# Performance work log

Measured on AMD Instinct MI355X. Metric: run time of the kernel, lower is better.

Reference implementation:

```python
import jax, jax.numpy as jnp
import numpy as np

B, S, H = 1, 2048, 1024          # batch, seq, hidden_size
INTER, K, DST, DTR = 2048, 4, 16, 64  # intermediate, kernel, ssm_state, dt_rank


def setup_inputs() -> dict:
    key = jax.random.key(0)
    ks = jax.random.split(key, 10)
    sc = 0.02
    return {
        "x": jax.random.normal(ks[0], (B, S, H), jnp.float32),
        "W_in": jax.random.normal(ks[1], (H, 2 * INTER), jnp.float32) * sc,
        "conv_w": jax.random.normal(ks[2], (K, 1, INTER), jnp.float32) * sc,
        "conv_b": jax.random.normal(ks[3], (INTER,), jnp.float32) * sc,
        "W_x": jax.random.normal(ks[4], (INTER, DTR + 2 * DST), jnp.float32) * sc,
        "W_dt": jax.random.normal(ks[5], (DTR, INTER), jnp.float32) * sc,
        "b_dt": jax.random.normal(ks[6], (INTER,), jnp.float32) * sc,
        "A_log": jax.random.normal(ks[7], (INTER, DST), jnp.float32) * sc,
        "D": jax.random.normal(ks[8], (INTER,), jnp.float32) * sc,
        "W_out": jax.random.normal(ks[9], (INTER, H), jnp.float32) * sc,
    }


def _ssm(dA, dBu, C):
    # dA, dBu: (b, s, h, d); C: (b, s, d) -> y: (b, s, h)
    xs = (jnp.moveaxis(dA, 1, 0), jnp.moveaxis(dBu, 1, 0), jnp.moveaxis(C, 1, 0))
    state0 = jnp.zeros(dA.shape[:1] + dA.shape[2:], dA.dtype)  # (b, h, d)

    def step(state, inp):
        Ai, dBui, Ci = inp  # (b,h,d), (b,h,d), (b,d)
        state = Ai * state + dBui
        y = jnp.einsum('bhd,bd->bh', state, Ci)
        return state, y

    _, ys = jax.lax.scan(step, state0, xs)  # ys: (s, b, h)
    return jnp.moveaxis(ys, 0, 1)


def reference(x, W_in, conv_w, conv_b, W_x, W_dt, b_dt, A_log, D, W_out):
    proj = x @ W_in                              # (b, s, 2*inter)
    raw, gate = jnp.split(proj, 2, axis=-1)      # each (b, s, inter)

    # causal depthwise conv over time, groups = inter
    conv = jax.lax.conv_general_dilated(
        raw, conv_w, window_strides=(1,), padding=[(K - 1, 0)],
        dimension_numbers=('NWC', 'WIO', 'NWC'), feature_group_count=INTER)
    h = jax.nn.silu(conv + conv_b)               # (b, s, inter)

    ssm_p = h @ W_x                              # (b, s, dtr + 2*d)
    ts, Bmat, C = jnp.split(ssm_p, [DTR, DTR + DST], axis=-1)
    dt = jax.nn.softplus(ts @ W_dt + b_dt)       # (b, s, inter)

    A = -jnp.exp(A_log)                          # (inter, d)
    dA = jnp.exp(dt[..., None] * A)              # (b, s, inter, d)
    dBu = dt[..., None] * Bmat[:, :, None, :] * h[..., None]  # (b, s, inter, d)

    y = _ssm(dA, dBu, C)                         # (b, s, inter)
    y = y + h * D
    y = y * jax.nn.silu(gate)
    return y @ W_out                             # (b, s, hidden)
```

## Files before the change

### kernel.cpp

```cpp
#include <hip/hip_runtime.h>
#include <math.h>

#define SEQ   2048
#define HID   1024
#define INTER 2048
#define DST   16
#define DTR   64
#define NP    96
#define NC    128
#define LCH   16
#define KS    16

typedef _Float16 f16;
typedef _Float16 f16x8 __attribute__((ext_vector_type(8)));
typedef _Float16 f16x4v __attribute__((ext_vector_type(4)));
typedef float f32x4 __attribute__((ext_vector_type(4)));

__device__ __forceinline__ float sigmoidf_(float x) { return 1.0f / (1.0f + expf(-x)); }
__device__ __forceinline__ float siluf_(float x)    { return x * sigmoidf_(x); }
__device__ __forceinline__ float softplusf_(float x){ return (x > 20.0f) ? x : log1pf(expf(x)); }

__device__ __forceinline__ int xcd_swz(int bid, int nwg)
{
    int cpx = nwg >> 3;
    return (bid & 7) * cpx + (bid >> 3);
}

__device__ __forceinline__ void tile_transpose(const float* __restrict__ W,
                                               f16* __restrict__ Wt,
                                               int K, int N, int bx, int by, int tid)
{
    __shared__ float t[32][33];
    const int n0 = bx * 32, k0 = by * 32;
    const int j = tid & 31, i0 = tid >> 5;
#pragma unroll
    for (int r = 0; r < 4; ++r)
        t[i0 + r * 8][j] = W[(size_t)(k0 + i0 + r * 8) * N + n0 + j];
    __syncthreads();
#pragma unroll
    for (int r = 0; r < 4; ++r)
        Wt[(size_t)(n0 + i0 + r * 8) * K + k0 + j] = (f16)t[j][i0 + r * 8];
}

__global__ __launch_bounds__(256) void prep_all(const float* __restrict__ x,
                                                const float* __restrict__ W_in,
                                                const float* __restrict__ W_out,
                                                const float* __restrict__ W_x,
                                                const float* __restrict__ W_dt,
                                                f16* __restrict__ xh,
                                                f16* __restrict__ W_in_t,
                                                f16* __restrict__ W_out_t,
                                                f16* __restrict__ WxT,
                                                f16* __restrict__ WdtT)
{
    const int bid = blockIdx.x, tid = threadIdx.x;
    if (bid < 2048) {
        int i = (bid * 256 + tid) * 4;
        float4 v = *(const float4*)&x[i];
        f16x4v o;
        o.x = (f16)v.x; o.y = (f16)v.y; o.z = (f16)v.z; o.w = (f16)v.w;
        *(f16x4v*)&xh[i] = o;
    } else if (bid < 6144) {
        int t = bid - 2048;
        tile_transpose(W_in, W_in_t, HID, 4096, t & 127, t >> 7, tid);
    } else if (bid < 8192) {
        int t = bid - 6144;
        tile_transpose(W_out, W_out_t, INTER, HID, t & 31, t >> 5, tid);
    } else if (bid < 8384) {
        int t = bid - 8192;
        tile_transpose(W_x, WxT, INTER, NP, t % 3, t / 3, tid);
    } else {
        int t = bid - 8384;
        tile_transpose(W_dt, WdtT, DTR, INTER, t & 63, t >> 6, tid);
    }
}

template<int BM, int BN, int KK, typename OutT>
__global__ __launch_bounds__(256) void gemm_f16mfma(const f16* __restrict__ Ah,
                                                    const f16* __restrict__ Bt,
                                                    OutT* __restrict__ C,
                                                    int N, int nbx)
{
    constexpr int BK = 64;
    __shared__ __align__(16) f16 As[BM * BK];
    __shared__ __align__(16) f16 Bs[BN * BK];

    const int tile = xcd_swz(blockIdx.x, gridDim.x);
    const int bx = tile % nbx, by = tile / nbx;

    const int tid = threadIdx.x;
    const int wid = tid >> 6, lane = tid & 63;
    const int wr = wid >> 1, wc = wid & 1;
    const int m0 = by * BM, n0 = bx * BN;
    const int l15 = lane & 15, lhi = lane >> 4;

    constexpr int MR = BM / 32;
    constexpr int NR = BN / 32;

    f32x4 acc[MR][NR] = {};

    for (int k0 = 0; k0 < KK; k0 += BK) {
        constexpr int CA = BM * BK * 2 / 1024;
#pragma unroll
        for (int c0 = 0; c0 < CA; c0 += 4) {
            int c = c0 + wid;
            int e = c * 64 + lane;
            int row = e >> 3, seg = e & 7;
            __builtin_amdgcn_global_load_lds(
                (const __attribute__((address_space(1))) unsigned int*)
                    (Ah + (size_t)(m0 + row) * KK + k0 + seg * 8),
                (__attribute__((address_space(3))) unsigned int*)(As + c * 512),
                16, 0, 0);
        }
        constexpr int CB = BN * BK * 2 / 1024;
#pragma unroll
        for (int c0 = 0; c0 < CB; c0 += 4) {
            int c = c0 + wid;
            int e = c * 64 + lane;
            int row = e >> 3, seg = e & 7;
            __builtin_amdgcn_global_load_lds(
                (const __attribute__((address_space(1))) unsigned int*)
                    (Bt + (size_t)(n0 + row) * KK + k0 + seg * 8),
                (__attribute__((address_space(3))) unsigned int*)(Bs + c * 512),
                16, 0, 0);
        }
        __syncthreads();

#pragma unroll
        for (int kk = 0; kk < BK; kk += 32) {
            f16x8 af[MR], bf[NR];
#pragma unroll
            for (int i = 0; i < MR; ++i)
                af[i] = *(const f16x8*)&As[(wr * (BM / 2) + i * 16 + l15) * BK + kk + lhi * 8];
#pragma unroll
            for (int n = 0; n < NR; ++n)
                bf[n] = *(const f16x8*)&Bs[(wc * (BN / 2) + n * 16 + l15) * BK + kk + lhi * 8];
#pragma unroll
            for (int i = 0; i < MR; ++i)
#pragma unroll
                for (int n = 0; n < NR; ++n)
                    acc[i][n] = __builtin_amdgcn_mfma_f32_16x16x32_f16(af[i], bf[n], acc[i][n], 0, 0, 0);
        }
        __syncthreads();
    }

#pragma unroll
    for (int i = 0; i < MR; ++i)
#pragma unroll
        for (int n = 0; n < NR; ++n)
#pragma unroll
            for (int r = 0; r < 4; ++r)
                C[(size_t)(m0 + wr * (BM / 2) + i * 16 + lhi * 4 + r) * N
                  + n0 + wc * (BN / 2) + n * 16 + l15] = (OutT)acc[i][n][r];
}

__global__ __launch_bounds__(256) void hwx_mfma(const f16* __restrict__ hh,
                                                const f16* __restrict__ WxT,
                                                f16* __restrict__ partials)
{
    constexpr int BM = 128, BN = 96, BK = 64;
    __shared__ __align__(16) f16 As[BM * BK];
    __shared__ __align__(16) f16 Bs[BN * BK];

    const int tile = xcd_swz(blockIdx.x, gridDim.x);
    const int bxm = tile & 15, ks = tile >> 4;

    const int tid = threadIdx.x;
    const int wid = tid >> 6, lane = tid & 63;
    const int wr = wid >> 1, wc = wid & 1;
    const int m0 = bxm * BM;
    const int l15 = lane & 15, lhi = lane >> 4;

    constexpr int MR = 4, NR = 3;
    f32x4 acc[MR][NR] = {};

    for (int k0 = ks * 128; k0 < ks * 128 + 128; k0 += BK) {
#pragma unroll
        for (int c0 = 0; c0 < 16; c0 += 4) {
            int c = c0 + wid;
            int e = c * 64 + lane;
            int row = e >> 3, seg = e & 7;
            __builtin_amdgcn_global_load_lds(
                (const __attribute__((address_space(1))) unsigned int*)
                    (hh + (size_t)(m0 + row) * INTER + k0 + seg * 8),
                (__attribute__((address_space(3))) unsigned int*)(As + c * 512),
                16, 0, 0);
        }
#pragma unroll
        for (int c0 = 0; c0 < 12; c0 += 4) {
            int c = c0 + wid;
            int e = c * 64 + lane;
            int row = e >> 3, seg = e & 7;
            __builtin_amdgcn_global_load_lds(
                (const __attribute__((address_space(1))) unsigned int*)
                    (WxT + (size_t)row * INTER + k0 + seg * 8),
                (__attribute__((address_space(3))) unsigned int*)(Bs + c * 512),
                16, 0, 0);
        }
        __syncthreads();

#pragma unroll
        for (int kk = 0; kk < BK; kk += 32) {
            f16x8 af[MR], bf[NR];
#pragma unroll
            for (int i = 0; i < MR; ++i)
                af[i] = *(const f16x8*)&As[(wr * 64 + i * 16 + l15) * BK + kk + lhi * 8];
#pragma unroll
            for (int n = 0; n < NR; ++n)
                bf[n] = *(const f16x8*)&Bs[(wc * 48 + n * 16 + l15) * BK + kk + lhi * 8];
#pragma unroll
            for (int i = 0; i < MR; ++i)
#pragma unroll
                for (int n = 0; n < NR; ++n)
                    acc[i][n] = __builtin_amdgcn_mfma_f32_16x16x32_f16(af[i], bf[n], acc[i][n], 0, 0, 0);
        }
        __syncthreads();
    }

    f16* P = partials + (size_t)ks * (SEQ * NP);
#pragma unroll
    for (int i = 0; i < MR; ++i)
#pragma unroll
        for (int n = 0; n < NR; ++n)
#pragma unroll
            for (int r = 0; r < 4; ++r)
                P[(size_t)(m0 + wr * 64 + i * 16 + lhi * 4 + r) * NP
                  + wc * 48 + n * 16 + l15] = (f16)acc[i][n][r];
}

__global__ __launch_bounds__(256) void reduce_partials(const f16* __restrict__ partials,
                                                       float* __restrict__ ssm_p,
                                                       f16* __restrict__ tsh)
{
    int t = blockIdx.x * 256 + threadIdx.x;
    int i8 = t * 8;
    int s = i8 / NP, j0 = i8 % NP;
    float a[8] = {};
#pragma unroll
    for (int c = 0; c < KS; ++c) {
        f16x8 v = *(const f16x8*)&partials[(size_t)c * (SEQ * NP) + i8];
#pragma unroll
        for (int j = 0; j < 8; ++j) a[j] += (float)v[j];
    }
    if (j0 < DTR) {
        f16x8 o;
#pragma unroll
        for (int j = 0; j < 8; ++j) o[j] = (f16)a[j];
        *(f16x8*)&tsh[(size_t)s * DTR + j0] = o;
    } else {
        *(float4*)&ssm_p[(size_t)s * NP + j0]     = make_float4(a[0], a[1], a[2], a[3]);
        *(float4*)&ssm_p[(size_t)s * NP + j0 + 4] = make_float4(a[4], a[5], a[6], a[7]);
    }
}

__global__ __launch_bounds__(256) void dt_mfma(const f16* __restrict__ tsh,
                                               const f16* __restrict__ WdtT,
                                               const float* __restrict__ bdt,
                                               f16* __restrict__ dtbh)
{
    constexpr int BM = 128, BN = 128, BK = 64;
    __shared__ __align__(16) f16 As[BM * BK];
    __shared__ __align__(16) f16 Bs[BN * BK];

    const int tile = xcd_swz(blockIdx.x, gridDim.x);
    const int bx = tile & 15, by = tile >> 4;

    const int tid = threadIdx.x;
    const int wid = tid >> 6, lane = tid & 63;
    const int wr = wid >> 1, wc = wid & 1;
    const int m0 = by * BM, n0 = bx * BN;
    const int l15 = lane & 15, lhi = lane >> 4;

    constexpr int MR = 4, NR = 4;
    f32x4 acc[MR][NR] = {};

#pragma unroll
    for (int c0 = 0; c0 < 16; c0 += 4) {
        int c = c0 + wid;
        int e = c * 64 + lane;
        int row = e >> 3, seg = e & 7;
        __builtin_amdgcn_global_load_lds(
            (const __attribute__((address_space(1))) unsigned int*)
                (tsh + (size_t)(m0 + row) * DTR + seg * 8),
            (__attribute__((address_space(3))) unsigned int*)(As + c * 512),
            16, 0, 0);
        __builtin_amdgcn_global_load_lds(
            (const __attribute__((address_space(1))) unsigned int*)
                (WdtT + (size_t)(n0 + row) * DTR + seg * 8),
            (__attribute__((address_space(3))) unsigned int*)(Bs + c * 512),
            16, 0, 0);
    }
    __syncthreads();

#pragma unroll
    for (int kk = 0; kk < 64; kk += 32) {
        f16x8 af[MR], bf[NR];
#pragma unroll
        for (int i = 0; i < MR; ++i)
            af[i] = *(const f16x8*)&As[(wr * 64 + i * 16 + l15) * BK + kk + lhi * 8];
#pragma unroll
        for (int n = 0; n < NR; ++n)
            bf[n] = *(const f16x8*)&Bs[(wc * 64 + n * 16 + l15) * BK + kk + lhi * 8];
#pragma unroll
        for (int i = 0; i < MR; ++i)
#pragma unroll
            for (int n = 0; n < NR; ++n)
                acc[i][n] = __builtin_amdgcn_mfma_f32_16x16x32_f16(af[i], bf[n], acc[i][n], 0, 0, 0);
    }

#pragma unroll
    for (int i = 0; i < MR; ++i)
#pragma unroll
        for (int n = 0; n < NR; ++n) {
            int col = n0 + wc * 64 + n * 16 + l15;
            float bv = bdt[col];
#pragma unroll
            for (int r = 0; r < 4; ++r)
                dtbh[(size_t)(m0 + wr * 64 + i * 16 + lhi * 4 + r) * INTER + col] =
                    (f16)softplusf_(acc[i][n][r] + bv);
        }
}

__global__ __launch_bounds__(256) void conv_silu(const f16* __restrict__ projh,
                                                 const float* __restrict__ cw,
                                                 const float* __restrict__ cb,
                                                 f16* __restrict__ hh)
{
    int idx = blockIdx.x * 256 + threadIdx.x;
    int c8 = (idx & (INTER / 8 - 1)) * 8;
    int s = idx >> 8;
    float acc[8];
#pragma unroll
    for (int j = 0; j < 8; ++j) acc[j] = cb[c8 + j];
#pragma unroll
    for (int k = 0; k < 4; ++k) {
        int sp = s + k - 3;
        if (sp >= 0) {
            f16x8 p = *(const f16x8*)&projh[(size_t)sp * (2 * INTER) + c8];
#pragma unroll
            for (int j = 0; j < 8; ++j)
                acc[j] = fmaf((float)p[j], cw[k * INTER + c8 + j], acc[j]);
        }
    }
    f16x8 o;
#pragma unroll
    for (int j = 0; j < 8; ++j) o[j] = (f16)siluf_(acc[j]);
    *(f16x8*)&hh[(size_t)idx * 8] = o;
}

__global__ __launch_bounds__(256) void ssm_pass1(const f16* __restrict__ dtbh,
                                                 const f16* __restrict__ hh,
                                                 const float* __restrict__ ssm_p,
                                                 const float* __restrict__ A_log,
                                                 float* __restrict__ Sbuf,
                                                 float* __restrict__ Pbuf)
{
    const int h = blockIdx.x * 256 + threadIdx.x;
    const int c = blockIdx.y;
    const int s0 = c * LCH;

    __shared__ float Bs[LCH][DST];
    for (int j = threadIdx.x; j < LCH * DST; j += 256) {
        int r = j >> 4, dd = j & 15;
        Bs[r][dd] = ssm_p[(size_t)(s0 + r) * NP + DTR + dd];
    }
    __syncthreads();

    float A[DST], st[DST];
#pragma unroll
    for (int d = 0; d < DST; ++d) {
        A[d] = -__expf(A_log[(size_t)h * DST + d]);
        st[d] = 0.0f;
    }

    float dtsum = 0.0f;
    for (int r = 0; r < LCH; ++r) {
        float dtv = (float)dtbh[(size_t)(s0 + r) * INTER + h];
        float hv  = (float)hh[(size_t)(s0 + r) * INTER + h];
        float dh = dtv * hv;
        dtsum += dtv;
#pragma unroll
        for (int d = 0; d < DST; ++d) {
            float da = __expf(dtv * A[d]);
            st[d] = fmaf(da, st[d], dh * Bs[r][d]);
        }
    }

    size_t base = ((size_t)c * INTER + h) * DST;
#pragma unroll
    for (int d = 0; d < DST; d += 4) {
        *(float4*)&Sbuf[base + d] = make_float4(st[d], st[d+1], st[d+2], st[d+3]);
        float4 p4;
        p4.x = __expf(A[d]     * dtsum);
        p4.y = __expf(A[d + 1] * dtsum);
        p4.z = __expf(A[d + 2] * dtsum);
        p4.w = __expf(A[d + 3] * dtsum);
        *(float4*)&Pbuf[base + d] = p4;
    }
}

__global__ __launch_bounds__(256) void ssm_pass2(const float* __restrict__ Sbuf,
                                                 const float* __restrict__ Pbuf,
                                                 float* __restrict__ Cin)
{
    int i = blockIdx.x * 256 + threadIdx.x;
    float carry = 0.0f;
#pragma unroll 8
    for (int c = 0; c < NC; ++c) {
        size_t idx = (size_t)c * (INTER * DST) + i;
        Cin[idx] = carry;
        carry = fmaf(Pbuf[idx], carry, Sbuf[idx]);
    }
}

__global__ __launch_bounds__(256) void ssm_pass3(const f16* __restrict__ dtbh,
                                                 const f16* __restrict__ hh,
                                                 const float* __restrict__ ssm_p,
                                                 const f16* __restrict__ projh,
                                                 const float* __restrict__ A_log,
                                                 const float* __restrict__ Dvec,
                                                 const float* __restrict__ Cin,
                                                 f16* __restrict__ yh)
{
    const int h = blockIdx.x * 256 + threadIdx.x;
    const int c = blockIdx.y;
    const int s0 = c * LCH;

    __shared__ float Bs[LCH][DST];
    __shared__ float Cs[LCH][DST];
    for (int j = threadIdx.x; j < LCH * DST; j += 256) {
        int r = j >> 4, dd = j & 15;
        Bs[r][dd] = ssm_p[(size_t)(s0 + r) * NP + DTR + dd];
        Cs[r][dd] = ssm_p[(size_t)(s0 + r) * NP + DTR + DST + dd];
    }
    __syncthreads();

    float A[DST], st[DST];
    size_t base = ((size_t)c * INTER + h) * DST;
#pragma unroll
    for (int d = 0; d < DST; ++d) {
        A[d] = -__expf(A_log[(size_t)h * DST + d]);
        st[d] = Cin[base + d];
    }
    const float Dv = Dvec[h];

    for (int r = 0; r < LCH; ++r) {
        float dtv = (float)dtbh[(size_t)(s0 + r) * INTER + h];
        float hv  = (float)hh[(size_t)(s0 + r) * INTER + h];
        float g   = (float)projh[(size_t)(s0 + r) * (2 * INTER) + INTER + h];
        float dh = dtv * hv;
        float y = 0.0f;
#pragma unroll
        for (int d = 0; d < DST; ++d) {
            float da = __expf(dtv * A[d]);
            st[d] = fmaf(da, st[d], dh * Bs[r][d]);
            y = fmaf(st[d], Cs[r][d], y);
        }
        y = fmaf(hv, Dv, y);
        yh[(size_t)(s0 + r) * INTER + h] = (f16)(y * siluf_(g));
    }
}

extern "C" void kernel_launch(void* const* d_in, const int* in_sizes, int n_in,
                              void* d_out, int out_size, void* d_ws, size_t ws_size,
                              hipStream_t stream)
{
    const float* x      = (const float*)d_in[0];
    const float* W_in   = (const float*)d_in[1];
    const float* conv_w = (const float*)d_in[2];
    const float* conv_b = (const float*)d_in[3];
    const float* W_x    = (const float*)d_in[4];
    const float* W_dt   = (const float*)d_in[5];
    const float* b_dt   = (const float*)d_in[6];
    const float* A_log  = (const float*)d_in[7];
    const float* Dv     = (const float*)d_in[8];
    const float* W_out  = (const float*)d_in[9];
    float* out = (float*)d_out;

    float* ws = (float*)d_ws;
    f16*  projh  = (f16*)ws;
    f16*  hh     = (f16*)(ws + 4194304);
    f16*  dtbh   = (f16*)(ws + 6291456);
    f16*  yh     = (f16*)(ws + 8388608);
    f16*  xh     = (f16*)(ws + 10485760);
    f16*  W_in_t = (f16*)(ws + 11534336);
    f16*  W_out_t= (f16*)(ws + 13631488);
    f16*  WxT    = (f16*)(ws + 14680064);
    f16*  tsh    = (f16*)(ws + 14778368);
    f16*  WdtT   = (f16*)(ws + 14843904);
    float* ssm_p = ws + 14909440;
    f16*  parts  = (f16*)(ws + 15106048);
    float* Sbuf  = ws + 16678912;
    float* Pbuf  = ws + 20873216;
    float* Cin   = ws + 25067520;

    prep_all<<<8512, 256, 0, stream>>>(x, W_in, W_out, W_x, W_dt,
                                       xh, W_in_t, W_out_t, WxT, WdtT);

    gemm_f16mfma<128, 128, HID, f16><<<512, 256, 0, stream>>>(
        xh, W_in_t, projh, 2 * INTER, 32);

    conv_silu<<<(SEQ * INTER / 8) / 256, 256, 0, stream>>>(projh, conv_w, conv_b, hh);

    hwx_mfma<<<256, 256, 0, stream>>>(hh, WxT, parts);
    reduce_partials<<<(SEQ * NP / 8) / 256, 256, 0, stream>>>(parts, ssm_p, tsh);

    dt_mfma<<<256, 256, 0, stream>>>(tsh, WdtT, b_dt, dtbh);

    ssm_pass1<<<dim3(INTER / 256, NC), 256, 0, stream>>>(dtbh, hh, ssm_p, A_log, Sbuf, Pbuf);
    ssm_pass2<<<(INTER * DST) / 256, 256, 0, stream>>>(Sbuf, Pbuf, Cin);
    ssm_pass3<<<dim3(INTER / 256, NC), 256, 0, stream>>>(dtbh, hh, ssm_p, projh, A_log, Dv, Cin, yh);

    gemm_f16mfma<64, 128, INTER, float><<<256, 256, 0, stream>>>(
        yh, W_out_t, out, HID, 8);
}
```

Baseline: 183.0 us.

## Split-K both projection GEMMs and fold partial reduction into conv and output passes

Both large GEMMs now use a split-K of 2, writing f16 partial planes, which doubles the number of workgroups (1024 and 512) so more compute units are filled. The in-projection partials are summed inside a new conv_gate kernel that also writes a separate gate buffer. The out-projection partials are summed by a new reduce_out kernel. The SSM chunking changes to 64 chunks of 32 steps. In exchange the partial planes add extra memory traffic, one extra launch, and an extra f16 rounding of the partial sums.

```diff
diff --git a/kernel.cpp b/kernel.cpp
--- a/kernel.cpp
+++ b/kernel.cpp
@@ -7,8 +7,8 @@
 #define DST   16
 #define DTR   64
 #define NP    96
-#define NC    128
-#define LCH   16
+#define NC    64
+#define LCH   32
 #define KS    16
 
 typedef _Float16 f16;
@@ -75,18 +75,21 @@
     }
 }
 
-template<int BM, int BN, int KK, typename OutT>
-__global__ __launch_bounds__(256) void gemm_f16mfma(const f16* __restrict__ Ah,
-                                                    const f16* __restrict__ Bt,
-                                                    OutT* __restrict__ C,
-                                                    int N, int nbx)
+template<int BM, int BN, int KTOT, int KCH>
+__global__ __launch_bounds__(256) void gemm_sk_f16(const f16* __restrict__ Ah,
+                                                   const f16* __restrict__ Bt,
+                                                   f16* __restrict__ planes,
+                                                   int N, int nbx, int nby)
 {
     constexpr int BK = 64;
     __shared__ __align__(16) f16 As[BM * BK];
     __shared__ __align__(16) f16 Bs[BN * BK];
 
     const int tile = xcd_swz(blockIdx.x, gridDim.x);
-    const int bx = tile % nbx, by = tile / nbx;
+    const int bx = tile % nbx;
+    const int rem = tile / nbx;
+    const int by = rem % nby;
+    const int ks = rem / nby;
 
     const int tid = threadIdx.x;
     const int wid = tid >> 6, lane = tid & 63;
@@ -99,7 +102,7 @@
 
     f32x4 acc[MR][NR] = {};
 
-    for (int k0 = 0; k0 < KK; k0 += BK) {
+    for (int k0 = ks * KCH; k0 < ks * KCH + KCH; k0 += BK) {
         constexpr int CA = BM * BK * 2 / 1024;
 #pragma unroll
         for (int c0 = 0; c0 < CA; c0 += 4) {
@@ -108,7 +111,7 @@
             int row = e >> 3, seg = e & 7;
             __builtin_amdgcn_global_load_lds(
                 (const __attribute__((address_space(1))) unsigned int*)
-                    (Ah + (size_t)(m0 + row) * KK + k0 + seg * 8),
+                    (Ah + (size_t)(m0 + row) * KTOT + k0 + seg * 8),
                 (__attribute__((address_space(3))) unsigned int*)(As + c * 512),
                 16, 0, 0);
         }
@@ -120,7 +123,7 @@
             int row = e >> 3, seg = e & 7;
             __builtin_amdgcn_global_load_lds(
                 (const __attribute__((address_space(1))) unsigned int*)
-                    (Bt + (size_t)(n0 + row) * KK + k0 + seg * 8),
+                    (Bt + (size_t)(n0 + row) * KTOT + k0 + seg * 8),
                 (__attribute__((address_space(3))) unsigned int*)(Bs + c * 512),
                 16, 0, 0);
         }
@@ -144,6 +147,7 @@
         __syncthreads();
     }
 
+    f16* C = planes + (size_t)ks * ((size_t)nby * BM * N);
 #pragma unroll
     for (int i = 0; i < MR; ++i)
 #pragma unroll
@@ -151,7 +155,48 @@
 #pragma unroll
             for (int r = 0; r < 4; ++r)
                 C[(size_t)(m0 + wr * (BM / 2) + i * 16 + lhi * 4 + r) * N
-                  + n0 + wc * (BN / 2) + n * 16 + l15] = (OutT)acc[i][n][r];
+                  + n0 + wc * (BN / 2) + n * 16 + l15] = (f16)acc[i][n][r];
+}
+
+__global__ __launch_bounds__(256) void conv_gate(const f16* __restrict__ pA,
+                                                 const float* __restrict__ cw,
+                                                 const float* __restrict__ cb,
+                                                 f16* __restrict__ hh,
+                                                 f16* __restrict__ gateh)
+{
+    const f16* p1 = pA + (size_t)SEQ * 4096;
+    int idx = blockIdx.x * 256 + threadIdx.x;
+    int cu = idx & 511;
+    int s = idx >> 9;
+    int col = cu * 8;
+    if (col < INTER) {
+        float acc[8];
+#pragma unroll
+        for (int j = 0; j < 8; ++j) acc[j] = cb[col + j];
+#pragma unroll
+        for (int k = 0; k < 4; ++k) {
+            int sp = s + k - 3;
+            if (sp >= 0) {
+                f16x8 a = *(const f16x8*)&pA[(size_t)sp * 4096 + col];
+                f16x8 b = *(const f16x8*)&p1[(size_t)sp * 4096 + col];
+#pragma unroll
+                for (int j = 0; j < 8; ++j)
+                    acc[j] = fmaf((float)a[j] + (float)b[j], cw[k * INTER + col + j], acc[j]);
+            }
+        }
+        f16x8 o;
+#pragma unroll
+        for (int j = 0; j < 8; ++j) o[j] = (f16)siluf_(acc[j]);
+        *(f16x8*)&hh[(size_t)s * INTER + col] = o;
+    } else {
+        int g = col - INTER;
+        f16x8 a = *(const f16x8*)&pA[(size_t)s * 4096 + col];
+        f16x8 b = *(const f16x8*)&p1[(size_t)s * 4096 + col];
+        f16x8 o;
+#pragma unroll
+        for (int j = 0; j < 8; ++j) o[j] = (f16)((float)a[j] + (float)b[j]);
+        *(f16x8*)&gateh[(size_t)s * INTER + g] = o;
+    }
 }
 
 __global__ __launch_bounds__(256) void hwx_mfma(const f16* __restrict__ hh,
@@ -321,33 +366,6 @@
         }
 }
 
-__global__ __launch_bounds__(256) void conv_silu(const f16* __restrict__ projh,
-                                                 const float* __restrict__ cw,
-                                                 const float* __restrict__ cb,
-                                                 f16* __restrict__ hh)
-{
-    int idx = blockIdx.x * 256 + threadIdx.x;
-    int c8 = (idx & (INTER / 8 - 1)) * 8;
-    int s = idx >> 8;
-    float acc[8];
-#pragma unroll
-    for (int j = 0; j < 8; ++j) acc[j] = cb[c8 + j];
-#pragma unroll
-    for (int k = 0; k < 4; ++k) {
-        int sp = s + k - 3;
-        if (sp >= 0) {
-            f16x8 p = *(const f16x8*)&projh[(size_t)sp * (2 * INTER) + c8];
-#pragma unroll
-            for (int j = 0; j < 8; ++j)
-                acc[j] = fmaf((float)p[j], cw[k * INTER + c8 + j], acc[j]);
-        }
-    }
-    f16x8 o;
-#pragma unroll
-    for (int j = 0; j < 8; ++j) o[j] = (f16)siluf_(acc[j]);
-    *(f16x8*)&hh[(size_t)idx * 8] = o;
-}
-
 __global__ __launch_bounds__(256) void ssm_pass1(const f16* __restrict__ dtbh,
                                                  const f16* __restrict__ hh,
                                                  const float* __restrict__ ssm_p,
@@ -416,7 +434,7 @@
 __global__ __launch_bounds__(256) void ssm_pass3(const f16* __restrict__ dtbh,
                                                  const f16* __restrict__ hh,
                                                  const float* __restrict__ ssm_p,
-                                                 const f16* __restrict__ projh,
+                                                 const f16* __restrict__ gateh,
                                                  const float* __restrict__ A_log,
                                                  const float* __restrict__ Dvec,
                                                  const float* __restrict__ Cin,
@@ -447,7 +465,7 @@
     for (int r = 0; r < LCH; ++r) {
         float dtv = (float)dtbh[(size_t)(s0 + r) * INTER + h];
         float hv  = (float)hh[(size_t)(s0 + r) * INTER + h];
-        float g   = (float)projh[(size_t)(s0 + r) * (2 * INTER) + INTER + h];
+        float g   = (float)gateh[(size_t)(s0 + r) * INTER + h];
         float dh = dtv * hv;
         float y = 0.0f;
 #pragma unroll
@@ -459,6 +477,25 @@
         y = fmaf(hv, Dv, y);
         yh[(size_t)(s0 + r) * INTER + h] = (f16)(y * siluf_(g));
     }
+}
+
+__global__ __launch_bounds__(256) void reduce_out(const f16* __restrict__ pY,
+                                                  float* __restrict__ out)
+{
+    int i8 = (blockIdx.x * 256 + threadIdx.x) * 8;
+    f16x8 a = *(const f16x8*)&pY[i8];
+    f16x8 b = *(const f16x8*)&pY[(size_t)SEQ * HID + i8];
+    float4 o1, o2;
+    o1.x = (float)a[0] + (float)b[0];
+    o1.y = (float)a[1] + (float)b[1];
+    o1.z = (float)a[2] + (float)b[2];
+    o1.w = (float)a[3] + (float)b[3];
+    o2.x = (float)a[4] + (float)b[4];
+    o2.y = (float)a[5] + (float)b[5];
+    o2.z = (float)a[6] + (float)b[6];
+    o2.w = (float)a[7] + (float)b[7];
+    *(float4*)&out[i8]     = o1;
+    *(float4*)&out[i8 + 4] = o2;
 }
 
 extern "C" void kernel_launch(void* const* d_in, const int* in_sizes, int n_in,
@@ -478,29 +515,31 @@
     float* out = (float*)d_out;
 
     float* ws = (float*)d_ws;
-    f16*  projh  = (f16*)ws;
-    f16*  hh     = (f16*)(ws + 4194304);
-    f16*  dtbh   = (f16*)(ws + 6291456);
-    f16*  yh     = (f16*)(ws + 8388608);
-    f16*  xh     = (f16*)(ws + 10485760);
-    f16*  W_in_t = (f16*)(ws + 11534336);
-    f16*  W_out_t= (f16*)(ws + 13631488);
-    f16*  WxT    = (f16*)(ws + 14680064);
-    f16*  tsh    = (f16*)(ws + 14778368);
-    f16*  WdtT   = (f16*)(ws + 14843904);
-    float* ssm_p = ws + 14909440;
-    f16*  parts  = (f16*)(ws + 15106048);
-    float* Sbuf  = ws + 16678912;
-    float* Pbuf  = ws + 20873216;
-    float* Cin   = ws + 25067520;
+    f16*  pA     = (f16*)ws;
+    f16*  hh     = (f16*)(ws + 8388608);
+    f16*  gateh  = (f16*)(ws + 10485760);
+    f16*  dtbh   = (f16*)(ws + 12582912);
+    f16*  yh     = (f16*)(ws + 14680064);
+    f16*  xh     = (f16*)(ws + 16777216);
+    f16*  W_in_t = (f16*)(ws + 17825792);
+    f16*  W_out_t= (f16*)(ws + 19922944);
+    f16*  WxT    = (f16*)(ws + 20971520);
+    f16*  tsh    = (f16*)(ws + 21069824);
+    f16*  WdtT   = (f16*)(ws + 21135360);
+    float* ssm_p = ws + 21200896;
+    f16*  parts  = (f16*)(ws + 21397504);
+    float* Sbuf  = ws + 22970368;
+    float* Pbuf  = ws + 25067520;
+    float* Cin   = ws + 27164672;
+    f16*  pY     = (f16*)(ws + 29261824);
 
     prep_all<<<8512, 256, 0, stream>>>(x, W_in, W_out, W_x, W_dt,
                                        xh, W_in_t, W_out_t, WxT, WdtT);
 
-    gemm_f16mfma<128, 128, HID, f16><<<512, 256, 0, stream>>>(
-        xh, W_in_t, projh, 2 * INTER, 32);
-
-    conv_silu<<<(SEQ * INTER / 8) / 256, 256, 0, stream>>>(projh, conv_w, conv_b, hh);
+    gemm_sk_f16<128, 128, HID, 512><<<1024, 256, 0, stream>>>(
+        xh, W_in_t, pA, 4096, 32, 16);
+
+    conv_gate<<<(SEQ * 4096 / 8) / 256, 256, 0, stream>>>(pA, conv_w, conv_b, hh, gateh);
 
     hwx_mfma<<<256, 256, 0, stream>>>(hh, WxT, parts);
     reduce_partials<<<(SEQ * NP / 8) / 256, 256, 0, stream>>>(parts, ssm_p, tsh);
@@ -509,8 +548,9 @@
 
     ssm_pass1<<<dim3(INTER / 256, NC), 256, 0, stream>>>(dtbh, hh, ssm_p, A_log, Sbuf, Pbuf);
     ssm_pass2<<<(INTER * DST) / 256, 256, 0, stream>>>(Sbuf, Pbuf, Cin);
-    ssm_pass3<<<dim3(INTER / 256, NC), 256, 0, stream>>>(dtbh, hh, ssm_p, projh, A_log, Dv, Cin, yh);
-
-    gemm_f16mfma<64, 128, INTER, float><<<256, 256, 0, stream>>>(
-        yh, W_out_t, out, HID, 8);
-}
+    ssm_pass3<<<dim3(INTER / 256, NC), 256, 0, stream>>>(dtbh, hh, ssm_p, gateh, A_log, Dv, Cin, yh);
+
+    gemm_sk_f16<64, 128, INTER, 1024><<<512, 256, 0, stream>>>(
+        yh, W_out_t, pY, HID, 8, 32);
+    reduce_out<<<(SEQ * HID / 8) / 256, 256, 0, stream>>>(pY, out);
+}
```

Result: no change. 183.9 us (+0.4%).
